# Performance work log

Measured on AMD Instinct MI355X. Metric: run time of the kernel, lower is better.

Reference implementation:

```python
import jax, jax.numpy as jnp
import numpy as np

ALPHA_LIM = (float(np.exp(-1.0 / 5.0)), float(np.exp(-1.0 / 25.0)))
BETA_LIM = (float(np.exp(-1.0 / 30.0)), float(np.exp(-1.0 / 120.0)))
A_LIM = (-1.0, 1.0)
B_LIM = (0.0, 2.0)
THRESHOLD = 1.0


@jax.custom_vjp
def spike_boxcar(x):
    # Heaviside forward, boxcar surrogate gradient
    return (x > 0).astype(x.dtype)


def _spike_fwd(x):
    return spike_boxcar(x), x


def _spike_bwd(x, g):
    return (jnp.where(jnp.abs(x) <= 0.5, g, jnp.zeros_like(g)),)


spike_boxcar.defvjp(_spike_fwd, _spike_bwd)


def setup_inputs() -> dict:
    key = jax.random.key(0)
    ks = jax.random.split(key, 9)
    B, T, I, H = 128, 512, 512, 512
    return {
        "x": jax.random.normal(ks[0], (B, T, I), dtype=jnp.float32),
        "W": jax.random.normal(ks[1], (H, I), dtype=jnp.float32) / np.sqrt(I),
        "alpha": jax.random.uniform(ks[2], (H,), dtype=jnp.float32),
        "beta": jax.random.uniform(ks[3], (H,), dtype=jnp.float32),
        "a": jax.random.uniform(ks[4], (H,), dtype=jnp.float32),
        "b": jax.random.uniform(ks[5], (H,), dtype=jnp.float32),
        "u0": jax.random.uniform(ks[6], (B, H), dtype=jnp.float32),
        "w0": jax.random.uniform(ks[7], (B, H), dtype=jnp.float32),
        "s0": jax.random.uniform(ks[8], (B, H), dtype=jnp.float32),
    }


def reference(x, W, alpha, beta, a, b, u0, w0, s0):
    # x: [B, T, I]; W: [H, I] (nn.Linear weight, no bias)
    alpha = jnp.clip(alpha, ALPHA_LIM[0], ALPHA_LIM[1])
    beta = jnp.clip(beta, BETA_LIM[0], BETA_LIM[1])
    a = jnp.clip(a, A_LIM[0], A_LIM[1])
    b = jnp.clip(b, B_LIM[0], B_LIM[1])

    Wx = jnp.einsum("bti,hi->bth", x, W)  # [B, T, H]
    Wx_t = jnp.transpose(Wx, (1, 0, 2))    # [T, B, H] for scan over time

    def step(carry, wx_t):
        ut, wt, st = carry
        wt = beta * wt + a * ut + b * st
        ut = alpha * (ut - st) + (1.0 - alpha) * (wx_t - wt)
        st = spike_boxcar(ut - THRESHOLD)
        return (ut, wt, st), st

    _, s = jax.lax.scan(step, (u0, w0, s0), Wx_t)  # s: [T, B, H]
    return jnp.transpose(s, (1, 0, 2))  # [B, T, H]
```

## Files before the change

kernel.cpp:

```cpp
#include <hip/hip_runtime.h>
#include <hip/hip_bf16.h>


#define M_SZ 65536
#define H_SZ 512
#define K_SZ 512
#define B_SZ 128
#define T_SZ 512
#define LSTR 132

typedef __attribute__((ext_vector_type(4))) float f32x4;

__device__ __forceinline__ bool detect_bf16(const unsigned int* __restrict__ w) {
  int c = 0;
#pragma unroll
  for (int i = 0; i < 64; ++i) {
    unsigned int e = (w[i] >> 7) & 0xffu;
    c += (e >= 115u && e <= 131u) ? 1 : 0;
  }
  return c > 32;
}

template <bool ISB>
__device__ __forceinline__ f32x4 ld4t(const void* __restrict__ p, size_t off) {
  if constexpr (!ISB) {
    return *reinterpret_cast<const f32x4*>(reinterpret_cast<const float*>(p) + off);
  } else {
    uint2 v = *reinterpret_cast<const uint2*>(reinterpret_cast<const unsigned short*>(p) + off);
    f32x4 r;
    r.x = __uint_as_float((v.x & 0xffffu) << 16);
    r.y = __uint_as_float(v.x & 0xffff0000u);
    r.z = __uint_as_float((v.y & 0xffffu) << 16);
    r.w = __uint_as_float(v.y & 0xffff0000u);
    return r;
  }
}

template <bool ISB>
__device__ __forceinline__ float ld1t(const void* __restrict__ p, int i) {
  if constexpr (!ISB) return reinterpret_cast<const float*>(p)[i];
  return __uint_as_float((unsigned int)(reinterpret_cast<const unsigned short*>(p)[i]) << 16);
}

template <bool ISB>
__device__ __forceinline__ void fused_body(
    const void* __restrict__ X, const void* __restrict__ Wm,
    const void* __restrict__ alpha_p, const void* __restrict__ beta_p,
    const void* __restrict__ a_p, const void* __restrict__ b_p,
    const void* __restrict__ u0p, const void* __restrict__ w0p,
    const void* __restrict__ s0p, void* __restrict__ out,
    float* __restrict__ As, float* __restrict__ Bs, float* __restrict__ st) {
  const int tid = threadIdx.x;
  const int r0 = tid >> 2;
  const int q0 = (tid & 3) * 4;
  const int tx = tid & 15;
  const int ty = tid >> 4;
  const int b = blockIdx.x >> 2;
  const int N0 = (blockIdx.x & 3) * 128;

  float* su = st;        float* sw = st + 128;  float* ss = st + 256;
  float* pal = st + 384; float* pbe = st + 512; float* pav = st + 640;
  float* pbv = st + 768; float* pom = st + 896;

  if (tid < 128) {
    const int h = N0 + tid;
    const float al = fminf(fmaxf(ld1t<ISB>(alpha_p, h), (float)0.8187307530779818),
                           (float)0.9607894391523232);
    const float be = fminf(fmaxf(ld1t<ISB>(beta_p, h), (float)0.9672161004820059),
                           (float)0.9917013044213351);
    pal[tid] = al;
    pbe[tid] = be;
    pav[tid] = fminf(fmaxf(ld1t<ISB>(a_p, h), -1.0f), 1.0f);
    pbv[tid] = fminf(fmaxf(ld1t<ISB>(b_p, h), 0.0f), 2.0f);
    pom[tid] = __fsub_rn(1.0f, al);
    const int bh = b * H_SZ + h;
    su[tid] = ld1t<ISB>(u0p, bh);
    sw[tid] = ld1t<ISB>(w0p, bh);
    ss[tid] = ld1t<ISB>(s0p, bh);
  }

  float* outf = reinterpret_cast<float*>(out);
  unsigned int* outu = reinterpret_cast<unsigned int*>(out);

  for (int tt = 0; tt < 4; ++tt) {
    const size_t M0 = (size_t)b * T_SZ + tt * 128;

    float acc[8][8];
#pragma unroll
    for (int i = 0; i < 8; ++i)
#pragma unroll
      for (int j = 0; j < 8; ++j) acc[i][j] = 0.0f;

    const size_t aoff0 = (M0 + r0) * K_SZ + q0;
    const size_t aoff1 = (M0 + r0 + 64) * K_SZ + q0;
    const size_t boff0 = (size_t)(N0 + r0) * K_SZ + q0;
    const size_t boff1 = (size_t)(N0 + r0 + 64) * K_SZ + q0;

    f32x4 pa0 = ld4t<ISB>(X, aoff0), pa1 = ld4t<ISB>(X, aoff1);
    f32x4 pb0 = ld4t<ISB>(Wm, boff0), pb1 = ld4t<ISB>(Wm, boff1);

    for (int kk = 0; kk < K_SZ; kk += 16) {
      __syncthreads();
      As[(q0 + 0) * LSTR + r0] = pa0.x; As[(q0 + 1) * LSTR + r0] = pa0.y;
      As[(q0 + 2) * LSTR + r0] = pa0.z; As[(q0 + 3) * LSTR + r0] = pa0.w;
      As[(q0 + 0) * LSTR + r0 + 64] = pa1.x; As[(q0 + 1) * LSTR + r0 + 64] = pa1.y;
      As[(q0 + 2) * LSTR + r0 + 64] = pa1.z; As[(q0 + 3) * LSTR + r0 + 64] = pa1.w;
      Bs[(q0 + 0) * LSTR + r0] = pb0.x; Bs[(q0 + 1) * LSTR + r0] = pb0.y;
      Bs[(q0 + 2) * LSTR + r0] = pb0.z; Bs[(q0 + 3) * LSTR + r0] = pb0.w;
      Bs[(q0 + 0) * LSTR + r0 + 64] = pb1.x; Bs[(q0 + 1) * LSTR + r0 + 64] = pb1.y;
      Bs[(q0 + 2) * LSTR + r0 + 64] = pb1.z; Bs[(q0 + 3) * LSTR + r0 + 64] = pb1.w;
      __syncthreads();
      if (kk + 16 < K_SZ) {
        pa0 = ld4t<ISB>(X, aoff0 + kk + 16); pa1 = ld4t<ISB>(X, aoff1 + kk + 16);
        pb0 = ld4t<ISB>(Wm, boff0 + kk + 16); pb1 = ld4t<ISB>(Wm, boff1 + kk + 16);
      }
#pragma unroll
      for (int k = 0; k < 16; ++k) {
        const f32x4 a0 = *reinterpret_cast<const f32x4*>(As + k * LSTR + ty * 4);
        const f32x4 a1 = *reinterpret_cast<const f32x4*>(As + k * LSTR + 64 + ty * 4);
        const f32x4 b0 = *reinterpret_cast<const f32x4*>(Bs + k * LSTR + tx * 4);
        const f32x4 b1 = *reinterpret_cast<const f32x4*>(Bs + k * LSTR + 64 + tx * 4);
        const float av[8] = {a0.x, a0.y, a0.z, a0.w, a1.x, a1.y, a1.z, a1.w};
        const float bv[8] = {b0.x, b0.y, b0.z, b0.w, b1.x, b1.y, b1.z, b1.w};
#pragma unroll
        for (int i = 0; i < 8; ++i)
#pragma unroll
          for (int j = 0; j < 8; ++j) acc[i][j] += av[i] * bv[j];
      }
    }

    for (int p = 0; p < 32; ++p) {
      const bool act = (p < 16) ? (ty == p) : (ty == p - 16);
      if (act) {
        float spkA[4][4];
        float spkB[4][4];
#pragma unroll
        for (int jj = 0; jj < 8; ++jj) {
          const int n = (jj < 4) ? (tx * 4 + jj) : (64 + tx * 4 + (jj - 4));
          float u = su[n], w = sw[n], s = ss[n];
          const float al = pal[n], be = pbe[n], av = pav[n], bv = pbv[n], om = pom[n];
#pragma unroll
          for (int rr = 0; rr < 4; ++rr) {
            const float cur = (p < 16) ? acc[rr][jj] : acc[4 + rr][jj];
            w = __fadd_rn(__fadd_rn(__fmul_rn(be, w), __fmul_rn(av, u)), __fmul_rn(bv, s));
            u = __fadd_rn(__fmul_rn(al, __fsub_rn(u, s)), __fmul_rn(om, __fsub_rn(cur, w)));
            s = (u > 1.0f) ? 1.0f : 0.0f;
            if (jj < 4) spkA[rr][jj] = s;
            else spkB[rr][jj - 4] = s;
          }
          su[n] = u; sw[n] = w; ss[n] = s;
        }
#pragma unroll
        for (int rr = 0; rr < 4; ++rr) {
          const size_t trow = ((size_t)b * T_SZ + tt * 128 + 4 * p + rr) * H_SZ + N0;
          if constexpr (!ISB) {
            f32x4 v0 = {spkA[rr][0], spkA[rr][1], spkA[rr][2], spkA[rr][3]};
            f32x4 v1 = {spkB[rr][0], spkB[rr][1], spkB[rr][2], spkB[rr][3]};
            *reinterpret_cast<f32x4*>(outf + trow + tx * 4) = v0;
            *reinterpret_cast<f32x4*>(outf + trow + 64 + tx * 4) = v1;
          } else {
            uint2 d0, d1;
            d0.x = (__float_as_uint(spkA[rr][1]) & 0xffff0000u) | (__float_as_uint(spkA[rr][0]) >> 16);
            d0.y = (__float_as_uint(spkA[rr][3]) & 0xffff0000u) | (__float_as_uint(spkA[rr][2]) >> 16);
            d1.x = (__float_as_uint(spkB[rr][1]) & 0xffff0000u) | (__float_as_uint(spkB[rr][0]) >> 16);
            d1.y = (__float_as_uint(spkB[rr][3]) & 0xffff0000u) | (__float_as_uint(spkB[rr][2]) >> 16);
            *reinterpret_cast<uint2*>(outu + (trow + tx * 4) / 2) = d0;
            *reinterpret_cast<uint2*>(outu + (trow + 64 + tx * 4) / 2) = d1;
          }
        }
      }
      __syncthreads();
    }
  }
}

__global__ __launch_bounds__(256) void adlif_fused(
    const void* __restrict__ X, const void* __restrict__ Wm,
    const void* __restrict__ alpha_p, const void* __restrict__ beta_p,
    const void* __restrict__ a_p, const void* __restrict__ b_p,
    const void* __restrict__ u0p, const void* __restrict__ w0p,
    const void* __restrict__ s0p, void* __restrict__ out) {
  __shared__ float As[16 * LSTR];
  __shared__ float Bs[16 * LSTR];
  __shared__ float st[8 * 128];
  if (detect_bf16(reinterpret_cast<const unsigned int*>(X)))
    fused_body<true>(X, Wm, alpha_p, beta_p, a_p, b_p, u0p, w0p, s0p, out, As, Bs, st);
  else
    fused_body<false>(X, Wm, alpha_p, beta_p, a_p, b_p, u0p, w0p, s0p, out, As, Bs, st);
}

extern "C" void kernel_launch(void* const* d_in, const int* in_sizes, int n_in,
                              void* d_out, int out_size, void* d_ws, size_t ws_size,
                              hipStream_t stream) {
  adlif_fused<<<dim3(B_SZ * 4), dim3(256), 0, stream>>>(
      d_in[0], d_in[1], d_in[2], d_in[3], d_in[4], d_in[5], d_in[6], d_in[7],
      d_in[8], d_out);
}
```

Measured before the change: 688.8 us.

## Stage GEMM tile in LDS and run recurrence per-thread with register state

Replaces the 32-phase serialized scan, where one ty-row of threads at a time advanced the recurrence with state in shared memory and a barrier per phase, with a staging scheme. The accumulator tile is written to a 32x128 LDS buffer in four chunks, then 128 threads each own one neuron and scan 32 timesteps with state and parameters held in registers. This cuts barriers from 32 to 8 per tile and removes shared-memory state traffic. The trade-off is that half the block sits idle during the scan and output stores become scalar per element, still coalesced across threads.

```diff
diff --git a/kernel.cpp b/kernel.cpp
--- a/kernel.cpp
+++ b/kernel.cpp
@@ -49,7 +49,7 @@
     const void* __restrict__ a_p, const void* __restrict__ b_p,
     const void* __restrict__ u0p, const void* __restrict__ w0p,
     const void* __restrict__ s0p, void* __restrict__ out,
-    float* __restrict__ As, float* __restrict__ Bs, float* __restrict__ st) {
+    float* __restrict__ As, float* __restrict__ Bs, float* __restrict__ wxs) {
   const int tid = threadIdx.x;
   const int r0 = tid >> 2;
   const int q0 = (tid & 3) * 4;
@@ -58,29 +58,24 @@
   const int b = blockIdx.x >> 2;
   const int N0 = (blockIdx.x & 3) * 128;
 
-  float* su = st;        float* sw = st + 128;  float* ss = st + 256;
-  float* pal = st + 384; float* pbe = st + 512; float* pav = st + 640;
-  float* pbv = st + 768; float* pom = st + 896;
-
+  float al = 0.f, be = 0.f, av = 0.f, bv = 0.f, om = 0.f, u = 0.f, w = 0.f, s = 0.f;
   if (tid < 128) {
     const int h = N0 + tid;
-    const float al = fminf(fmaxf(ld1t<ISB>(alpha_p, h), (float)0.8187307530779818),
-                           (float)0.9607894391523232);
-    const float be = fminf(fmaxf(ld1t<ISB>(beta_p, h), (float)0.9672161004820059),
-                           (float)0.9917013044213351);
-    pal[tid] = al;
-    pbe[tid] = be;
-    pav[tid] = fminf(fmaxf(ld1t<ISB>(a_p, h), -1.0f), 1.0f);
-    pbv[tid] = fminf(fmaxf(ld1t<ISB>(b_p, h), 0.0f), 2.0f);
-    pom[tid] = __fsub_rn(1.0f, al);
+    al = fminf(fmaxf(ld1t<ISB>(alpha_p, h), (float)0.8187307530779818),
+               (float)0.9607894391523232);
+    be = fminf(fmaxf(ld1t<ISB>(beta_p, h), (float)0.9672161004820059),
+               (float)0.9917013044213351);
+    av = fminf(fmaxf(ld1t<ISB>(a_p, h), -1.0f), 1.0f);
+    bv = fminf(fmaxf(ld1t<ISB>(b_p, h), 0.0f), 2.0f);
+    om = __fsub_rn(1.0f, al);
     const int bh = b * H_SZ + h;
-    su[tid] = ld1t<ISB>(u0p, bh);
-    sw[tid] = ld1t<ISB>(w0p, bh);
-    ss[tid] = ld1t<ISB>(s0p, bh);
+    u = ld1t<ISB>(u0p, bh);
+    w = ld1t<ISB>(w0p, bh);
+    s = ld1t<ISB>(s0p, bh);
   }
 
   float* outf = reinterpret_cast<float*>(out);
-  unsigned int* outu = reinterpret_cast<unsigned int*>(out);
+  unsigned short* outu = reinterpret_cast<unsigned short*>(out);
 
   for (int tt = 0; tt < 4; ++tt) {
     const size_t M0 = (size_t)b * T_SZ + tt * 128;
@@ -120,56 +115,46 @@
         const f32x4 a1 = *reinterpret_cast<const f32x4*>(As + k * LSTR + 64 + ty * 4);
         const f32x4 b0 = *reinterpret_cast<const f32x4*>(Bs + k * LSTR + tx * 4);
         const f32x4 b1 = *reinterpret_cast<const f32x4*>(Bs + k * LSTR + 64 + tx * 4);
-        const float av[8] = {a0.x, a0.y, a0.z, a0.w, a1.x, a1.y, a1.z, a1.w};
-        const float bv[8] = {b0.x, b0.y, b0.z, b0.w, b1.x, b1.y, b1.z, b1.w};
+        const float avv[8] = {a0.x, a0.y, a0.z, a0.w, a1.x, a1.y, a1.z, a1.w};
+        const float bvv[8] = {b0.x, b0.y, b0.z, b0.w, b1.x, b1.y, b1.z, b1.w};
 #pragma unroll
         for (int i = 0; i < 8; ++i)
 #pragma unroll
-          for (int j = 0; j < 8; ++j) acc[i][j] += av[i] * bv[j];
+          for (int j = 0; j < 8; ++j) acc[i][j] += avv[i] * bvv[j];
       }
     }
-
-    for (int p = 0; p < 32; ++p) {
-      const bool act = (p < 16) ? (ty == p) : (ty == p - 16);
-      if (act) {
-        float spkA[4][4];
-        float spkB[4][4];
 #pragma unroll
-        for (int jj = 0; jj < 8; ++jj) {
-          const int n = (jj < 4) ? (tx * 4 + jj) : (64 + tx * 4 + (jj - 4));
-          float u = su[n], w = sw[n], s = ss[n];
-          const float al = pal[n], be = pbe[n], av = pav[n], bv = pbv[n], om = pom[n];
-#pragma unroll
-          for (int rr = 0; rr < 4; ++rr) {
-            const float cur = (p < 16) ? acc[rr][jj] : acc[4 + rr][jj];
-            w = __fadd_rn(__fadd_rn(__fmul_rn(be, w), __fmul_rn(av, u)), __fmul_rn(bv, s));
-            u = __fadd_rn(__fmul_rn(al, __fsub_rn(u, s)), __fmul_rn(om, __fsub_rn(cur, w)));
-            s = (u > 1.0f) ? 1.0f : 0.0f;
-            if (jj < 4) spkA[rr][jj] = s;
-            else spkB[rr][jj - 4] = s;
-          }
-          su[n] = u; sw[n] = w; ss[n] = s;
-        }
+    for (int sub = 0; sub < 4; ++sub) {
+      __syncthreads();
+      const bool owner = (sub & 1) ? (ty >= 8) : (ty < 8);
+      if (owner) {
 #pragma unroll
         for (int rr = 0; rr < 4; ++rr) {
-          const size_t trow = ((size_t)b * T_SZ + tt * 128 + 4 * p + rr) * H_SZ + N0;
-          if constexpr (!ISB) {
-            f32x4 v0 = {spkA[rr][0], spkA[rr][1], spkA[rr][2], spkA[rr][3]};
-            f32x4 v1 = {spkB[rr][0], spkB[rr][1], spkB[rr][2], spkB[rr][3]};
-            *reinterpret_cast<f32x4*>(outf + trow + tx * 4) = v0;
-            *reinterpret_cast<f32x4*>(outf + trow + 64 + tx * 4) = v1;
-          } else {
-            uint2 d0, d1;
-            d0.x = (__float_as_uint(spkA[rr][1]) & 0xffff0000u) | (__float_as_uint(spkA[rr][0]) >> 16);
-            d0.y = (__float_as_uint(spkA[rr][3]) & 0xffff0000u) | (__float_as_uint(spkA[rr][2]) >> 16);
-            d1.x = (__float_as_uint(spkB[rr][1]) & 0xffff0000u) | (__float_as_uint(spkB[rr][0]) >> 16);
-            d1.y = (__float_as_uint(spkB[rr][3]) & 0xffff0000u) | (__float_as_uint(spkB[rr][2]) >> 16);
-            *reinterpret_cast<uint2*>(outu + (trow + tx * 4) / 2) = d0;
-            *reinterpret_cast<uint2*>(outu + (trow + 64 + tx * 4) / 2) = d1;
-          }
+          const int row = (ty & 7) * 4 + rr;
+          const int r = (sub < 2) ? rr : 4 + rr;
+          f32x4 v0 = {acc[r][0], acc[r][1], acc[r][2], acc[r][3]};
+          f32x4 v1 = {acc[r][4], acc[r][5], acc[r][6], acc[r][7]};
+          *reinterpret_cast<f32x4*>(wxs + row * 128 + tx * 4) = v0;
+          *reinterpret_cast<f32x4*>(wxs + row * 128 + 64 + tx * 4) = v1;
         }
       }
       __syncthreads();
+      if (tid < 128) {
+        const size_t tbase =
+            ((size_t)b * T_SZ + tt * 128 + sub * 32) * H_SZ + N0 + tid;
+#pragma unroll
+        for (int t = 0; t < 32; ++t) {
+          const float cur = wxs[t * 128 + tid];
+          w = __fadd_rn(__fadd_rn(__fmul_rn(be, w), __fmul_rn(av, u)), __fmul_rn(bv, s));
+          u = __fadd_rn(__fmul_rn(al, __fsub_rn(u, s)), __fmul_rn(om, __fsub_rn(cur, w)));
+          const bool sp = (u > 1.0f);
+          s = sp ? 1.0f : 0.0f;
+          if constexpr (ISB)
+            outu[tbase + (size_t)t * H_SZ] = sp ? (unsigned short)0x3F80u : (unsigned short)0u;
+          else
+            outf[tbase + (size_t)t * H_SZ] = s;
+        }
+      }
     }
   }
 }
@@ -182,11 +167,11 @@
     const void* __restrict__ s0p, void* __restrict__ out) {
   __shared__ float As[16 * LSTR];
   __shared__ float Bs[16 * LSTR];
-  __shared__ float st[8 * 128];
+  __shared__ float wxs[32 * 128];
   if (detect_bf16(reinterpret_cast<const unsigned int*>(X)))
-    fused_body<true>(X, Wm, alpha_p, beta_p, a_p, b_p, u0p, w0p, s0p, out, As, Bs, st);
+    fused_body<true>(X, Wm, alpha_p, beta_p, a_p, b_p, u0p, w0p, s0p, out, As, Bs, wxs);
   else
-    fused_body<false>(X, Wm, alpha_p, beta_p, a_p, b_p, u0p, w0p, s0p, out, As, Bs, st);
+    fused_body<false>(X, Wm, alpha_p, beta_p, a_p, b_p, u0p, w0p, s0p, out, As, Bs, wxs);
 }
 
 extern "C" void kernel_launch(void* const* d_in, const int* in_sizes, int n_in,
```

Result: faster. 591.0 us (-14.2%).
